# Performance work log

Measured on AMD Instinct MI355X. Metric: run time of the kernel, lower is better.

Reference implementation:

```python
import jax, jax.numpy as jnp
import numpy as np

B, T, I, H = 64, 512, 512, 512

def setup_inputs() -> dict:
    key = jax.random.key(0)
    k1, k2, k3, k4, k5 = jax.random.split(key, 5)
    stdv = 1.0 / np.sqrt(H)
    return {
        "x": jax.random.normal(k1, (B, T, I), dtype=jnp.float32),
        "h0": jax.random.normal(k2, (B, H), dtype=jnp.float32),
        "U_i": jax.random.uniform(k3, (I, H), minval=-stdv, maxval=stdv, dtype=jnp.float32),
        "V_i": jax.random.uniform(k4, (H, H), minval=-stdv, maxval=stdv, dtype=jnp.float32),
        "b_i": jax.random.uniform(k5, (H,), minval=-stdv, maxval=stdv, dtype=jnp.float32),
    }

def reference(x, h0, U_i, V_i, b_i):
    # Precompute the input projection for all timesteps as one big GEMM: [B,T,H]
    xU = jnp.einsum("bti,ih->bth", x, U_i) + b_i
    # Sequential recurrence over time with lax.scan (time-major carry)
    def step(h, xU_t):
        h_new = jnp.tanh(xU_t + h @ V_i)  # [B,H]
        return h_new, h_new
    _, hs = jax.lax.scan(step, h0, jnp.swapaxes(xU, 0, 1))  # hs: [T,B,H]
    return jnp.swapaxes(hs, 0, 1)  # [B,T,H]
```

## Files before the change

### kernel.cpp

```cpp
#include <hip/hip_runtime.h>
#include <hip/hip_bf16.h>

#define Bsz 64
#define Tsz 512
#define Isz 512
#define Hsz 512

__global__ __launch_bounds__(256) void p1_gemm(const float* __restrict__ X,
                                               const float* __restrict__ U,
                                               const float* __restrict__ bias,
                                               float* __restrict__ out) {
  const int K = Isz, N = Hsz;
  __shared__ float As[32][128];
  __shared__ float Bs[32][64];
  const int MB = (Bsz * Tsz) / 128;
  int bm = blockIdx.x & (MB - 1);
  int bn = blockIdx.x >> 8;
  int t = threadIdx.x;
  int tx = t & 15, ty = t >> 4;

  float acc[8][4];
#pragma unroll
  for (int r = 0; r < 8; r++)
#pragma unroll
    for (int c = 0; c < 4; c++) acc[r][c] = 0.f;

  const float* Xb = X + (size_t)bm * 128 * K;
  const float* Ub = U + bn * 64;

  for (int k0 = 0; k0 < K; k0 += 32) {
    int ar = t >> 3, aq = t & 7;
#pragma unroll
    for (int i = 0; i < 4; i++) {
      int row = ar + 32 * i;
      float4 v = *(const float4*)&Xb[(size_t)row * K + k0 + 4 * aq];
      As[4 * aq + 0][row] = v.x;
      As[4 * aq + 1][row] = v.y;
      As[4 * aq + 2][row] = v.z;
      As[4 * aq + 3][row] = v.w;
    }
    int bkk = t >> 4, bq = t & 15;
#pragma unroll
    for (int i = 0; i < 2; i++) {
      int kk = bkk + 16 * i;
      *(float4*)&Bs[kk][4 * bq] = *(const float4*)&Ub[(size_t)(k0 + kk) * N + 4 * bq];
    }
    __syncthreads();
#pragma unroll
    for (int kk = 0; kk < 32; kk++) {
      float4 A0 = *(const float4*)&As[kk][ty * 8];
      float4 A1 = *(const float4*)&As[kk][ty * 8 + 4];
      float4 B0 = *(const float4*)&Bs[kk][tx * 4];
      float av[8] = {A0.x, A0.y, A0.z, A0.w, A1.x, A1.y, A1.z, A1.w};
      float bv[4] = {B0.x, B0.y, B0.z, B0.w};
#pragma unroll
      for (int r = 0; r < 8; r++)
#pragma unroll
        for (int c = 0; c < 4; c++) acc[r][c] += av[r] * bv[c];
    }
    __syncthreads();
  }

  float4 bias4 = *(const float4*)&bias[bn * 64 + tx * 4];
  float bb[4] = {bias4.x, bias4.y, bias4.z, bias4.w};
#pragma unroll
  for (int r = 0; r < 8; r++) {
    float4 o;
    o.x = acc[r][0] + bb[0];
    o.y = acc[r][1] + bb[1];
    o.z = acc[r][2] + bb[2];
    o.w = acc[r][3] + bb[3];
    *(float4*)&out[((size_t)bm * 128 + ty * 8 + r) * N + bn * 64 + tx * 4] = o;
  }
}

#define NGrp 32
#define BPGrp 8
#define CPB 64
#define HOFFS (CPB * Hsz)

__device__ __forceinline__ float ftanh(float x) {
  float ax = fabsf(x);
  float e = __expf(2.f * ax);
  float r = 1.f - 2.f / (e + 1.f);
  return copysignf(r, x);
}

__device__ __forceinline__ int hswz(int k) { return k ^ (((k >> 6) & 7) << 2); }

__device__ __forceinline__ unsigned long long packha(float h, int tag) {
  return (unsigned long long)__float_as_uint(h) |
         ((unsigned long long)(unsigned)tag << 32);
}

__global__ __launch_bounds__(512) void p2_rnn(
    const float* __restrict__ h0, const float* __restrict__ V,
    float* __restrict__ out, unsigned long long* __restrict__ atoms) {
  extern __shared__ float sm[];
  float4* __restrict__ Vl = (float4*)sm;
  float* __restrict__ hsm = sm + HOFFS;

  int bid = blockIdx.x;
  int g = bid & 31;
  int jb = bid >> 5;
  int t = threadIdx.x;
  int c = t >> 3, ks = t & 7;
  int w = t >> 6, cl = c & 7;

  for (int rep = 0; rep < 64; rep++) {
    int idx = rep * 512 + t;
    int row = idx >> 6, cc = idx & 63;
    float val = V[(size_t)row * Hsz + CPB * jb + cc];
    int ksr = row >> 6, ir = (row >> 2) & 15, jr = row & 3;
    sm[(cc >> 3) * 4096 + ir * 256 + ksr * 32 + (cc & 7) * 4 + jr] = val;
  }
  {
    int k = t;
    hsm[hswz(k)] = h0[(size_t)(2 * g + 0) * Hsz + k];
    hsm[512 + hswz(k)] = h0[(size_t)(2 * g + 1) * Hsz + k];
  }
  __syncthreads();

  bool owner = (ks == 0);
  int col = CPB * jb + c;
  size_t ob0 = ((size_t)(2 * g + 0) * Tsz) * Hsz + col;
  size_t ob1 = ((size_t)(2 * g + 1) * Tsz) * Hsz + col;
  float xu0 = 0.f, xu1 = 0.f;
  if (owner) { xu0 = out[ob0]; xu1 = out[ob1]; }

  const int vbase = w * 1024 + ks * 8 + cl;
  const int swk = ks << 2;
  const int hb = ks * 64;
  const int pk = t;

  for (int s = 0; s < Tsz; s++) {
    float xn0 = 0.f, xn1 = 0.f;
    if (owner && s + 1 < Tsz) {
      xn0 = out[ob0 + (size_t)(s + 1) * Hsz];
      xn1 = out[ob1 + (size_t)(s + 1) * Hsz];
    }

    float a00 = 0.f, a01 = 0.f, a02 = 0.f, a03 = 0.f;
    float a10 = 0.f, a11 = 0.f, a12 = 0.f, a13 = 0.f;
#pragma unroll
    for (int i = 0; i < 16; i++) {
      float4 v = Vl[vbase + i * 64];
      int hf = hb + ((4 * i) ^ swk);
      float4 hA = *(const float4*)&hsm[hf];
      float4 hB = *(const float4*)&hsm[512 + hf];
      a00 += v.x * hA.x; a01 += v.y * hA.y; a02 += v.z * hA.z; a03 += v.w * hA.w;
      a10 += v.x * hB.x; a11 += v.y * hB.y; a12 += v.z * hB.z; a13 += v.w * hB.w;
    }
    float r0 = (a00 + a01) + (a02 + a03);
    float r1 = (a10 + a11) + (a12 + a13);
    r0 += __shfl_xor(r0, 1); r0 += __shfl_xor(r0, 2); r0 += __shfl_xor(r0, 4);
    r1 += __shfl_xor(r1, 1); r1 += __shfl_xor(r1, 2); r1 += __shfl_xor(r1, 4);

    int p = (s + 1) & 1;
    if (owner) {
      float h0v = ftanh(r0 + xu0);
      float h1v = ftanh(r1 + xu1);
      out[ob0 + (size_t)s * Hsz] = h0v;
      out[ob1 + (size_t)s * Hsz] = h1v;
      if (s + 1 < Tsz) {
        __hip_atomic_store(&atoms[((size_t)p * Bsz + 2 * g + 0) * Hsz + col],
                           packha(h0v, s + 1), __ATOMIC_RELAXED,
                           __HIP_MEMORY_SCOPE_AGENT);
        __hip_atomic_store(&atoms[((size_t)p * Bsz + 2 * g + 1) * Hsz + col],
                           packha(h1v, s + 1), __ATOMIC_RELAXED,
                           __HIP_MEMORY_SCOPE_AGENT);
      }
    }
    xu0 = xn0; xu1 = xn1;

    if (s + 1 < Tsz) {
      __syncthreads();
      unsigned long long* q0 = &atoms[((size_t)p * Bsz + 2 * g + 0) * Hsz + pk];
      unsigned long long* q1 = &atoms[((size_t)p * Bsz + 2 * g + 1) * Hsz + pk];
      int want = s + 1;
      float hv0 = 0.f, hv1 = 0.f;
      bool d0 = false, d1 = false;
      int guard = 0;
      while (true) {
        if (!d0) {
          unsigned long long a = __hip_atomic_load(q0, __ATOMIC_RELAXED,
                                                   __HIP_MEMORY_SCOPE_AGENT);
          if ((int)(a >> 32) == want) { hv0 = __uint_as_float((unsigned)a); d0 = true; }
        }
        if (!d1) {
          unsigned long long a = __hip_atomic_load(q1, __ATOMIC_RELAXED,
                                                   __HIP_MEMORY_SCOPE_AGENT);
          if ((int)(a >> 32) == want) { hv1 = __uint_as_float((unsigned)a); d1 = true; }
        }
        if (d0 && d1) break;
        if (++guard > (1 << 20)) break;
      }
      hsm[hswz(pk)] = hv0;
      hsm[512 + hswz(pk)] = hv1;
      __syncthreads();
    }
  }
}

extern "C" void kernel_launch(void* const* d_in, const int* in_sizes, int n_in,
                              void* d_out, int out_size, void* d_ws, size_t ws_size,
                              hipStream_t stream) {
  const float* x  = (const float*)d_in[0];
  const float* h0 = (const float*)d_in[1];
  const float* U  = (const float*)d_in[2];
  const float* V  = (const float*)d_in[3];
  const float* b  = (const float*)d_in[4];
  float* out = (float*)d_out;
  unsigned long long* atoms = (unsigned long long*)d_ws;

  static const int kDynLds = (HOFFS + 2 * Hsz) * 4;
  hipFuncSetAttribute(reinterpret_cast<const void*>(p2_rnn),
                      hipFuncAttributeMaxDynamicSharedMemorySize, kDynLds);

  p1_gemm<<<dim3(2048), dim3(256), 0, stream>>>(x, U, b, out);

  p2_rnn<<<dim3(256), dim3(512), kDynLds, stream>>>(h0, V, out, atoms);
}
```

Baseline: 1.472 ms.

## Restructure RNN recurrence: 32-way K split, DPP reductions, double-buffered h

The per-step matvec is remapped so each thread covers 16 K-rows for 4 columns and both batch rows, with V stored in LDS as swizzled float4 and h interleaved as float2 pairs. The cross-lane reduction now uses DPP and ds_swizzle instead of shuffles. h is double-buffered in LDS, which removes one __syncthreads per timestep. The intent is to cut the per-step latency of the serial recurrence; the costs are a longer 32-lane reduction tree and more complex indexing.

Measured after the change: 1.355 ms. 1.09x faster.

```diff
diff --git a/kernel.cpp b/kernel.cpp
--- a/kernel.cpp
+++ b/kernel.cpp
@@ -77,7 +77,6 @@
 #define NGrp 32
 #define BPGrp 8
 #define CPB 64
-#define HOFFS (CPB * Hsz)
 
 __device__ __forceinline__ float ftanh(float x) {
   float ax = fabsf(x);
@@ -86,95 +85,106 @@
   return copysignf(r, x);
 }
 
-__device__ __forceinline__ int hswz(int k) { return k ^ (((k >> 6) & 7) << 2); }
+template <int CTRL>
+__device__ __forceinline__ float dppadd(float x) {
+  int y = __builtin_amdgcn_update_dpp(0, __float_as_int(x), CTRL, 0xf, 0xf, true);
+  return x + __int_as_float(y);
+}
+__device__ __forceinline__ float swz16add(float x) {
+  return x + __int_as_float(
+                 __builtin_amdgcn_ds_swizzle(__float_as_int(x), 0x401F));
+}
+
+__device__ __forceinline__ int fh(int k) {
+  int ks = k >> 4, kp = (k >> 1) & 7, e = k & 1;
+  return (ks << 5) + (((kp ^ (ks & 7))) << 2) + (e << 1);
+}
 
 __device__ __forceinline__ unsigned long long packha(float h, int tag) {
   return (unsigned long long)__float_as_uint(h) |
          ((unsigned long long)(unsigned)tag << 32);
 }
 
-__global__ __launch_bounds__(512) void p2_rnn(
+__global__ __launch_bounds__(512, 2) void p2_rnn(
     const float* __restrict__ h0, const float* __restrict__ V,
     float* __restrict__ out, unsigned long long* __restrict__ atoms) {
   extern __shared__ float sm[];
   float4* __restrict__ Vl = (float4*)sm;
-  float* __restrict__ hsm = sm + HOFFS;
+  float* __restrict__ hsm = sm + 32768;
 
   int bid = blockIdx.x;
   int g = bid & 31;
   int jb = bid >> 5;
   int t = threadIdx.x;
-  int c = t >> 3, ks = t & 7;
-  int w = t >> 6, cl = c & 7;
-
-  for (int rep = 0; rep < 64; rep++) {
+  int cq = t >> 5, ks = t & 31;
+
+  for (int rep = 0; rep < 16; rep++) {
     int idx = rep * 512 + t;
-    int row = idx >> 6, cc = idx & 63;
-    float val = V[(size_t)row * Hsz + CPB * jb + cc];
-    int ksr = row >> 6, ir = (row >> 2) & 15, jr = row & 3;
-    sm[(cc >> 3) * 4096 + ir * 256 + ksr * 32 + (cc & 7) * 4 + jr] = val;
+    int k = idx >> 4, cg = idx & 15;
+    float4 gv = *(const float4*)&V[(size_t)k * Hsz + CPB * jb + 4 * cg];
+    Vl[k * 16 + (cg ^ ((k >> 4) & 15))] = gv;
   }
   {
     int k = t;
-    hsm[hswz(k)] = h0[(size_t)(2 * g + 0) * Hsz + k];
-    hsm[512 + hswz(k)] = h0[(size_t)(2 * g + 1) * Hsz + k];
+    float2 hv;
+    hv.x = h0[(size_t)(2 * g + 0) * Hsz + k];
+    hv.y = h0[(size_t)(2 * g + 1) * Hsz + k];
+    *(float2*)&hsm[fh(k)] = hv;
   }
   __syncthreads();
 
-  bool owner = (ks == 0);
-  int col = CPB * jb + c;
-  size_t ob0 = ((size_t)(2 * g + 0) * Tsz) * Hsz + col;
-  size_t ob1 = ((size_t)(2 * g + 1) * Tsz) * Hsz + col;
-  float xu0 = 0.f, xu1 = 0.f;
-  if (owner) { xu0 = out[ob0]; xu1 = out[ob1]; }
-
-  const int vbase = w * 1024 + ks * 8 + cl;
-  const int swk = ks << 2;
-  const int hb = ks * 64;
+  bool own = (ks < 8);
+  int ob = ks >> 2, jj = ks & 3;
+  int col = CPB * jb + cq * 4 + jj;
+  size_t obase = ((size_t)(2 * g + ob) * Tsz) * Hsz + col;
+  float xu = own ? out[obase] : 0.f;
+
+  const int cs = cq ^ (ks & 15);
+  const int k7 = ks & 7;
   const int pk = t;
 
   for (int s = 0; s < Tsz; s++) {
-    float xn0 = 0.f, xn1 = 0.f;
-    if (owner && s + 1 < Tsz) {
-      xn0 = out[ob0 + (size_t)(s + 1) * Hsz];
-      xn1 = out[ob1 + (size_t)(s + 1) * Hsz];
-    }
-
-    float a00 = 0.f, a01 = 0.f, a02 = 0.f, a03 = 0.f;
-    float a10 = 0.f, a11 = 0.f, a12 = 0.f, a13 = 0.f;
-#pragma unroll
-    for (int i = 0; i < 16; i++) {
-      float4 v = Vl[vbase + i * 64];
-      int hf = hb + ((4 * i) ^ swk);
-      float4 hA = *(const float4*)&hsm[hf];
-      float4 hB = *(const float4*)&hsm[512 + hf];
-      a00 += v.x * hA.x; a01 += v.y * hA.y; a02 += v.z * hA.z; a03 += v.w * hA.w;
-      a10 += v.x * hB.x; a11 += v.y * hB.y; a12 += v.z * hB.z; a13 += v.w * hB.w;
-    }
-    float r0 = (a00 + a01) + (a02 + a03);
-    float r1 = (a10 + a11) + (a12 + a13);
-    r0 += __shfl_xor(r0, 1); r0 += __shfl_xor(r0, 2); r0 += __shfl_xor(r0, 4);
-    r1 += __shfl_xor(r1, 1); r1 += __shfl_xor(r1, 2); r1 += __shfl_xor(r1, 4);
+    float xun = 0.f;
+    if (own && s + 1 < Tsz) xun = out[obase + (size_t)(s + 1) * Hsz];
+
+    const float* hp = &hsm[(s & 1) * 1024 + (ks << 5)];
+    const float4* vp = &Vl[(ks << 8) + cs];
+
+    float aA0 = 0, aA1 = 0, aA2 = 0, aA3 = 0;
+    float aB0 = 0, aB1 = 0, aB2 = 0, aB3 = 0;
+#pragma unroll
+    for (int kp = 0; kp < 8; kp++) {
+      float4 h4 = *(const float4*)&hp[(kp ^ k7) << 2];
+      float4 v0 = vp[kp * 32];
+      float4 v1 = vp[kp * 32 + 16];
+      aA0 += v0.x * h4.x + v1.x * h4.z;  aB0 += v0.x * h4.y + v1.x * h4.w;
+      aA1 += v0.y * h4.x + v1.y * h4.z;  aB1 += v0.y * h4.y + v1.y * h4.w;
+      aA2 += v0.z * h4.x + v1.z * h4.z;  aB2 += v0.z * h4.y + v1.z * h4.w;
+      aA3 += v0.w * h4.x + v1.w * h4.z;  aB3 += v0.w * h4.y + v1.w * h4.w;
+    }
+#define RED(x)                 \
+  x = dppadd<0xB1>(x);         \
+  x = dppadd<0x4E>(x);         \
+  x = dppadd<0x124>(x);        \
+  x = dppadd<0x128>(x);        \
+  x = swz16add(x);
+    RED(aA0) RED(aA1) RED(aA2) RED(aA3) RED(aB0) RED(aB1) RED(aB2) RED(aB3)
+#undef RED
 
     int p = (s + 1) & 1;
-    if (owner) {
-      float h0v = ftanh(r0 + xu0);
-      float h1v = ftanh(r1 + xu1);
-      out[ob0 + (size_t)s * Hsz] = h0v;
-      out[ob1 + (size_t)s * Hsz] = h1v;
-      if (s + 1 < Tsz) {
-        __hip_atomic_store(&atoms[((size_t)p * Bsz + 2 * g + 0) * Hsz + col],
-                           packha(h0v, s + 1), __ATOMIC_RELAXED,
+    if (own) {
+      float sum = ob ? ((jj & 2) ? ((jj & 1) ? aB3 : aB2) : ((jj & 1) ? aB1 : aB0))
+                     : ((jj & 2) ? ((jj & 1) ? aA3 : aA2) : ((jj & 1) ? aA1 : aA0));
+      float hv = ftanh(sum + xu);
+      out[obase + (size_t)s * Hsz] = hv;
+      if (s + 1 < Tsz)
+        __hip_atomic_store(&atoms[((size_t)p * Bsz + 2 * g + ob) * Hsz + col],
+                           packha(hv, s + 1), __ATOMIC_RELAXED,
                            __HIP_MEMORY_SCOPE_AGENT);
-        __hip_atomic_store(&atoms[((size_t)p * Bsz + 2 * g + 1) * Hsz + col],
-                           packha(h1v, s + 1), __ATOMIC_RELAXED,
-                           __HIP_MEMORY_SCOPE_AGENT);
-      }
-    }
-    xu0 = xn0; xu1 = xn1;
+      xu = xun;
+    }
 
     if (s + 1 < Tsz) {
-      __syncthreads();
       unsigned long long* q0 = &atoms[((size_t)p * Bsz + 2 * g + 0) * Hsz + pk];
       unsigned long long* q1 = &atoms[((size_t)p * Bsz + 2 * g + 1) * Hsz + pk];
       int want = s + 1;
@@ -195,8 +205,8 @@
         if (d0 && d1) break;
         if (++guard > (1 << 20)) break;
       }
-      hsm[hswz(pk)] = hv0;
-      hsm[512 + hswz(pk)] = hv1;
+      float2 hv; hv.x = hv0; hv.y = hv1;
+      *(float2*)&hsm[p * 1024 + fh(pk)] = hv;
       __syncthreads();
     }
   }
@@ -213,7 +223,7 @@
   float* out = (float*)d_out;
   unsigned long long* atoms = (unsigned long long*)d_ws;
 
-  static const int kDynLds = (HOFFS + 2 * Hsz) * 4;
+  static const int kDynLds = (32768 + 2 * 1024) * 4;
   hipFuncSetAttribute(reinterpret_cast<const void*>(p2_rnn),
                       hipFuncAttributeMaxDynamicSharedMemorySize, kDynLds);
 
```
